# Performance work log

Hardware: AMD Instinct MI355X
Metric: run time of the kernel (lower is better)

The kernel has to match this reference:

```python
import jax, jax.numpy as jnp
import numpy as np
import math

B, NS, NT = 8, 512, 512
NSRC, NTRG = B * NS, B * NT
E = 32768
SCALAR_DIM, EMBED, ORI, LAYERS, K, KK = 20, 128, 1024, 3, 5, 25
CONV_IN = 2 * EMBED
FINAL_IN = ORI + LAYERS * EMBED


def sinusoidal_pos_emb(x):
    half = SCALAR_DIM // 2
    freqs = jnp.exp(-(math.log(10000.0) / (half - 1)) * jnp.arange(half, dtype=x.dtype))
    ang = x[:, None] * freqs[None, :]
    return jnp.concatenate([jnp.sin(ang), jnp.cos(ang)], axis=-1)


def spline_basis(pseudo):
    # open B-spline basis, degree 1, kernel_size K per dim, dim=2 (torch_spline_conv semantics)
    v = pseudo * (K - 1)
    lo = jnp.floor(v)
    frac = v - lo
    lo = lo.astype(jnp.int32)
    idxs, ws = [], []
    for s1 in (0, 1):
        for s0 in (0, 1):
            i0 = jnp.clip(lo[:, 0] + s0, 0, K - 1)
            i1 = jnp.clip(lo[:, 1] + s1, 0, K - 1)
            w0 = frac[:, 0] if s0 else 1.0 - frac[:, 0]
            w1 = frac[:, 1] if s1 else 1.0 - frac[:, 1]
            idxs.append(i0 + K * i1)
            ws.append(w0 * w1)
    idx = jnp.stack(idxs, 1)  # [E,4] kernel indices
    w = jnp.stack(ws, 1)      # [E,4] basis weights
    e = pseudo.shape[0]
    # dense [E,KK] coefficient matrix (<=4 nonzeros per row)
    return jnp.zeros((e, KK), pseudo.dtype).at[jnp.arange(e)[:, None], idx].add(w)


def spline_conv(x, edge_index, edge_attr, W, root, bias):
    # SplineConv(in=CONV_IN, out=EMBED, dim=2, kernel_size=5, degree=1, aggr='mean', root_weight=True)
    src, dst = edge_index[0], edge_index[1]
    x_j = x[src]                    # [E, in] gather of source features
    C = spline_basis(edge_attr)     # [E, KK]
    msg = jnp.zeros((x_j.shape[0], W.shape[-1]), x.dtype)
    for k in range(KK):             # fixed small kernel loop (25 GEMMs)
        msg = msg + (C[:, k:k + 1] * x_j) @ W[k]
    n = x.shape[0]
    agg = jax.ops.segment_sum(msg, dst, num_segments=n)
    deg = jax.ops.segment_sum(jnp.ones((msg.shape[0],), x.dtype), dst, num_segments=n)
    agg = agg / jnp.clip(deg, 1.0)[:, None]   # mean aggregation
    return agg + x @ root + bias


def masked_softmax(src, mask):
    out = jnp.where(mask, src, -jnp.inf)
    out = jax.nn.softmax(out, axis=-1)
    return jnp.where(mask, out, 0.0)


def setup_inputs() -> dict:
    key = jax.random.key(0)
    ks = jax.random.split(key, 16)
    s = 0.02
    # block-diagonal edges: both endpoints within the same graph
    gs = jax.random.randint(ks[11], (E,), 0, B)
    gt = jax.random.randint(ks[12], (E,), 0, B)
    ei_s = jnp.stack([gs * NS + jax.random.randint(ks[13], (E,), 0, NS),
                      gs * NS + jax.random.randint(ks[14], (E,), 0, NS)])
    ei_t = jnp.stack([gt * NT + jax.random.randint(ks[15], (E,), 0, NT),
                      gt * NT + jax.random.randint(ks[0], (E,), 0, NT)])
    return {
        "t": jax.random.uniform(ks[1], (B,)),
        "Xt": jax.random.uniform(ks[2], (B, NS, NT)),
        "x_s": jax.random.normal(ks[3], (NSRC, ORI)),
        "x_t": jax.random.normal(ks[4], (NTRG, ORI)),
        "ea_s": jax.random.uniform(ks[5], (E, 2)),
        "ea_t": jax.random.uniform(ks[6], (E, 2)),
        "lin0_w": jax.random.normal(ks[7], (ORI + 2 * SCALAR_DIM, EMBED)) * s,
        "lin0_b": jnp.zeros((EMBED,)),
        "lin_w": jax.random.normal(ks[8], (LAYERS - 1, EMBED + 2 * SCALAR_DIM, EMBED)) * s,
        "lin_b": jnp.zeros((LAYERS - 1, EMBED)),
        "conv_w": jax.random.normal(ks[9], (LAYERS, KK, CONV_IN, EMBED)) * s,
        "conv_root": jax.random.normal(ks[10], (LAYERS, CONV_IN, EMBED)) * s,
        "conv_bias": jnp.zeros((LAYERS, EMBED)),
        "final_w": jax.random.normal(jax.random.fold_in(key, 99), (FINAL_IN, EMBED)) * s,
        "final_b": jnp.zeros((EMBED,)),
        "ei_s": ei_s,
        "ei_t": ei_t,
        "s_mask": jnp.ones((B, NS), dtype=bool),
        "t_mask": jnp.ones((B, NT), dtype=bool),
        "mask_align": jnp.ones((B, NS, NT), dtype=bool),
    }


def reference(t, Xt, x_s, x_t, ea_s, ea_t, lin0_w, lin0_b, lin_w, lin_b,
              conv_w, conv_root, conv_bias, final_w, final_b,
              ei_s, ei_t, s_mask, t_mask, mask_align):
    # All graphs have exactly NS/NT nodes, so s_mask/t_mask are all-True:
    # boolean select x[s_mask] == reshape, and to_dense_batch == reshape.
    time_emb = sinusoidal_pos_emb(t)                                    # [B, 20]
    num_src = sinusoidal_pos_emb(Xt.sum(-1).reshape(-1) / 10.0)         # [NSRC, 20]
    num_trg = sinusoidal_pos_emb(jnp.swapaxes(Xt, 1, 2).sum(-1).reshape(-1) / 10.0)
    tf_src = jnp.repeat(time_emb, NS, axis=0)                           # per-node time features
    tf_trg = jnp.repeat(time_emb, NT, axis=0)
    xs_src, xs_trg = [x_s], [x_t]
    for i in range(LAYERS):
        w = lin0_w if i == 0 else lin_w[i - 1]
        b = lin0_b if i == 0 else lin_b[i - 1]
        xin_s = jnp.concatenate([xs_src[-1], num_src, tf_src], -1) @ w + b
        xin_t = jnp.concatenate([xs_trg[-1], num_trg, tf_trg], -1) @ w + b
        xp_s = xin_s.reshape(B, NS, EMBED)
        xp_t = xin_t.reshape(B, NT, EMBED)
        tgt_msg = jnp.einsum('bst,btd->bsd', Xt, xp_t)
        src_msg = jnp.einsum('bst,bsd->btd', Xt, xp_s)
        diff_s = (xp_s - tgt_msg).reshape(NSRC, EMBED)
        diff_t = (xp_t - src_msg).reshape(NTRG, EMBED)
        cat_s = jnp.concatenate([xin_s, diff_s], -1)
        cat_t = jnp.concatenate([xin_t, diff_t], -1)
        xs_src.append(jnp.tanh(spline_conv(cat_s, ei_s, ea_s, conv_w[i], conv_root[i], conv_bias[i])))
        xs_trg.append(jnp.tanh(spline_conv(cat_t, ei_t, ea_t, conv_w[i], conv_root[i], conv_bias[i])))
    h_s = jnp.concatenate(xs_src, -1) @ final_w + final_b
    h_t = jnp.concatenate(xs_trg, -1) @ final_w + final_b
    sim = jnp.einsum('bsd,btd->bst', h_s.reshape(B, NS, EMBED), h_t.reshape(B, NT, EMBED))
    return masked_softmax(sim, mask_align).reshape(NSRC, NT)
```

## Files before the change

kernel.cpp:

```cpp
#include <hip/hip_runtime.h>
#include <hip/hip_bf16.h>

typedef __hip_bfloat16 hb;
typedef short short8 __attribute__((ext_vector_type(8)));
typedef float f32x4 __attribute__((ext_vector_type(4)));
typedef unsigned short u16;

#define NNODE 4096
#define NEDGE 32768
#define EMB   128
#define ORI   1024
#define SD    20
#define CIN   256
#define NCV   3328

__device__ __forceinline__ float b2f(hb v){ return __bfloat162float(v); }
__device__ __forceinline__ hb f2b(float v){ return __float2bfloat16(v); }

__device__ __forceinline__ void split2(float x, u16& hi, u16& lo){
  hb h = f2b(x);
  float r = x - b2f(h);
  hb l = f2b(r);
  __builtin_memcpy(&hi, &h, 2);
  __builtin_memcpy(&lo, &l, 2);
}

__device__ __forceinline__ void gl16(const void* g, void* l){
  __builtin_amdgcn_global_load_lds(
      (const __attribute__((address_space(1))) unsigned int*)(size_t)g,
      (__attribute__((address_space(3))) unsigned int*)(unsigned int)(size_t)l,
      16, 0, 0);
}


__global__ __launch_bounds__(256) void k_rowsum(const float* __restrict__ Xt, float* __restrict__ rowsum){
  int row = blockIdx.x*4 + (threadIdx.x >> 6);
  int lane = threadIdx.x & 63;
  const float* p = Xt + (size_t)row*512;
  float s = 0.f;
  for (int i = lane; i < 512; i += 64) s += p[i];
  for (int off = 32; off; off >>= 1) s += __shfl_xor(s, off);
  if (lane == 0) rowsum[row] = s;
}

__global__ __launch_bounds__(256) void k_colsum(const float* __restrict__ Xt, float* __restrict__ colsum){
  int col = blockIdx.x*256 + threadIdx.x;
  int b = col >> 9, t = col & 511;
  const float* p = Xt + (size_t)b*512*512 + t;
  float s = 0.f;
  for (int sidx = 0; sidx < 512; ++sidx) s += p[(size_t)sidx*512];
  colsum[col] = s;
}

__global__ void k_posemb(const float* __restrict__ vals, int n, float scale, float* __restrict__ out){
  int i = blockIdx.x*blockDim.x + threadIdx.x;
  if (i >= n) return;
  float x = vals[i]*scale;
  float c = -logf(10000.f)/9.f;
  for (int j = 0; j < 10; ++j) {
    float f = expf(c*(float)j);
    out[i*20 + j]      = sinf(x*f);
    out[i*20 + 10 + j] = cosf(x*f);
  }
}

__global__ void k_basis2(const float* __restrict__ ea_s, const float* __restrict__ ea_t,
                         int* __restrict__ idx4, float* __restrict__ w4){
  int e = blockIdx.x*256 + threadIdx.x;
  const float* ea = (e < NEDGE) ? ea_s : ea_t;
  int el = e & (NEDGE-1);
  float p0 = ea[el*2]   * 4.0f;
  float p1 = ea[el*2+1] * 4.0f;
  float l0 = floorf(p0), l1 = floorf(p1);
  float f0 = p0 - l0, f1 = p1 - l1;
  int i0 = (int)l0, i1 = (int)l1;
  int j = 0;
  for (int s1 = 0; s1 <= 1; ++s1)
    for (int s0 = 0; s0 <= 1; ++s0) {
      int a  = min(max(i0 + s0, 0), 4);
      int bb = min(max(i1 + s1, 0), 4);
      float w = (s0 ? f0 : 1.f - f0) * (s1 ? f1 : 1.f - f1);
      idx4[e*4 + j] = a + 5*bb;
      w4[e*4 + j] = w;
      ++j;
    }
}

__global__ void k_count2(const int* __restrict__ ds, const int* __restrict__ dt, int* __restrict__ cnt){
  int e = blockIdx.x*256 + threadIdx.x;
  int side = e >= NEDGE;
  int el = e & (NEDGE-1);
  int node = (side ? dt : ds)[el];
  atomicAdd(&cnt[side*NNODE + node], 1);
}

__global__ __launch_bounds__(256) void k_scan2(const int* __restrict__ cntAll, int* __restrict__ rowptrAll,
                                               int* __restrict__ eposAll, float* __restrict__ invAll){
  int sideOff = blockIdx.x*NNODE;
  const int* cnt = cntAll + sideOff;
  int* rowptr = rowptrAll + blockIdx.x*(NNODE+1);
  int* epos = eposAll + sideOff;
  float* inv = invAll + sideOff;
  __shared__ int part[256];
  int tid = threadIdx.x;
  int base = tid*16;
  int v[16]; int s = 0;
  #pragma unroll
  for (int i = 0; i < 16; ++i){
    v[i] = s; int c = cnt[base+i]; s += c;
    inv[base+i] = 1.f / fmaxf((float)c, 1.f);
  }
  part[tid] = s; __syncthreads();
  int total = s;
  for (int off = 1; off < 256; off <<= 1){
    int y = (tid >= off) ? part[tid-off] : 0;
    __syncthreads();
    part[tid] += y;
    __syncthreads();
  }
  int excl = part[tid] - total;
  #pragma unroll
  for (int i = 0; i < 16; ++i){ int r = excl + v[i]; rowptr[base+i] = r; epos[base+i] = r; }
  if (tid == 255) rowptr[4096] = part[255];
}

__global__ void k_fill2(const int* __restrict__ ds, const int* __restrict__ dt,
                        int* __restrict__ eposAll, int* __restrict__ elistAll){
  int e = blockIdx.x*256 + threadIdx.x;
  int side = e >= NEDGE;
  int el = e & (NEDGE-1);
  int node = (side ? dt : ds)[el];
  int p = atomicAdd(&eposAll[side*NNODE + node], 1);
  elistAll[side*NEDGE + p] = el;
}

__global__ __launch_bounds__(256) void k_xtT2(const float* __restrict__ Xt,
    u16* __restrict__ XH, u16* __restrict__ XL, u16* __restrict__ TH, u16* __restrict__ TL){
  __shared__ float tile[64][65];
  int b = blockIdx.z, s0 = blockIdx.y*64, t0 = blockIdx.x*64;
  const float* src = Xt + (size_t)b*262144;
  size_t ob = (size_t)b*262144;
  #pragma unroll 4
  for (int p = 0; p < 16; ++p) {
    int idx = p*256 + threadIdx.x;
    int r = idx >> 6, c = idx & 63;
    float v = src[(size_t)(s0+r)*512 + t0 + c];
    tile[r][c] = v;
    size_t o = ob + (size_t)(s0+r)*512 + t0 + c;
    split2(v, XH[o], XL[o]);
  }
  __syncthreads();
  #pragma unroll 4
  for (int p = 0; p < 16; ++p) {
    int idx = p*256 + threadIdx.x;
    int r = idx >> 6, c = idx & 63;
    float v = tile[c][r];
    size_t o = ob + (size_t)(t0+r)*512 + s0 + c;
    split2(v, TH[o], TL[o]);
  }
}

__global__ void k_wT2(const float* __restrict__ src, u16* __restrict__ dH, u16* __restrict__ dL,
                      int Krows, int ldDst){
  int i = blockIdx.x*256 + threadIdx.x;
  if (i >= 128*ldDst) return;
  int n = i / ldDst, k = i - n*ldDst;
  float v = (k < Krows) ? src[(size_t)k*128 + n] : 0.f;
  split2(v, dH[i], dL[i]);
}

__global__ void k_wc2(const float* __restrict__ convw, const float* __restrict__ root,
                      u16* __restrict__ dH, u16* __restrict__ dL){
  int i = blockIdx.x*256 + threadIdx.x;
  int l = i / (NCV*CIN);
  int r = i - l*(NCV*CIN);
  int k = r & 255, n = r >> 8;
  const float* cw = convw + (size_t)l*25*CIN*128;
  const float* rt = root  + (size_t)l*CIN*128;
  float v;
  if (n < 3200) { int kk = n >> 7, col = n & 127; v = cw[((size_t)kk*256 + k)*128 + col]; }
  else          { int col = n & 127;              v = rt[(size_t)k*128 + col]; }
  split2(v, dH[i], dL[i]);
}

__global__ void k_aux2(const float* __restrict__ nums, const float* __restrict__ numt,
                       const float* __restrict__ temb, u16* __restrict__ aH, u16* __restrict__ aL){
  int i = blockIdx.x*256 + threadIdx.x;
  if (i >= 8192*64) return;
  int r = i >> 6, c = i & 63;
  int side = r >> 12, local = r & 4095, b = (r >> 9) & 7;
  float v = 0.f;
  if (c < 20) v = (side ? numt : nums)[local*20 + c];
  else if (c < 40) v = temb[b*20 + (c - 20)];
  split2(v, aH[i], aL[i]);
}

__global__ __launch_bounds__(256) void k_split(const float* __restrict__ src,
    u16* __restrict__ dH, u16* __restrict__ dL, int n){
  int i = blockIdx.x*256 + threadIdx.x;
  if (i < n) split2(src[i], dH[i], dL[i]);
}

__global__ __launch_bounds__(256) void k_xinT(const float* __restrict__ src,
    u16* __restrict__ dH, u16* __restrict__ dL, float* __restrict__ cat){
  __shared__ float tile[64][65];
  int r0 = blockIdx.x*64, c0 = blockIdx.y*64;
  #pragma unroll 4
  for (int p = 0; p < 16; ++p) {
    int idx = p*256 + threadIdx.x;
    int r = idx >> 6, c = idx & 63;
    float v = src[(size_t)(r0+r)*128 + c0 + c];
    tile[r][c] = v;
    cat[(size_t)(r0+r)*256 + c0 + c]       = v;
    cat[(size_t)(r0+r)*256 + 128 + c0 + c] = v;
  }
  __syncthreads();
  #pragma unroll 4
  for (int p = 0; p < 16; ++p) {
    int idx = p*256 + threadIdx.x;
    int r = idx >> 6, c = idx & 63;
    float v = tile[c][r];
    size_t o = (size_t)(c0+r)*8192 + r0 + c;
    split2(v, dH[o], dL[o]);
  }
}

__global__ __launch_bounds__(256) void k_fillbias(const float* __restrict__ b, float* __restrict__ o){
  int i = blockIdx.x*256 + threadIdx.x;
  o[i] = b[i & 127];
}

__global__ __launch_bounds__(256) void k_gemm(
    const u16* __restrict__ Ah, const u16* __restrict__ Al, int lda, long aBatch,
    const u16* __restrict__ Bh, const u16* __restrict__ Bl, int ldb, long bBatch,
    int K, int flags, int ksplit,
    float* __restrict__ outF, const float* __restrict__ bias,
    int ldo, int oRowOff, int oBatchRows, const float* __restrict__ X,
    const u16* __restrict__ A2h, const u16* __restrict__ A2l,
    const u16* __restrict__ B2h, const u16* __restrict__ B2l, int oRowOff2)
{
  __shared__ __align__(16) u16 S[2][4][4096];
  const int tid = threadIdx.x;
  const int ln = tid & 63, w = tid >> 6;
  const int wm = (w >> 1)*64, wn = (w & 1)*64;
  const int l15 = ln & 15, q = ln >> 4;
  const int by = blockIdx.y;
  int bz = blockIdx.z;
  const u16* Aph = Ah; const u16* Apl = Al;
  const u16* Bph = Bh; const u16* Bpl = Bl;
  int rowOffSel = oRowOff;
  if (B2h != nullptr) {
    int half = gridDim.z >> 1;
    if (bz >= half) { bz -= half; Aph = A2h; Apl = A2l; Bph = B2h; Bpl = B2l; rowOffSel = oRowOff2; }
  }
  const int batch = bz / ksplit;
  const int kidx  = bz - batch*ksplit;
  const int bxm = blockIdx.x;
  const int kSteps = K >> 5;
  const int spc = (kSteps + ksplit - 1) / ksplit;
  const int kBeg = kidx * spc * 32;
  const int kEnd = min(K, kBeg + spc*32);
  if (kBeg >= kEnd) return;
  const u16* Abh = Aph + (size_t)batch*aBatch + (size_t)bxm*128*lda;
  const u16* Abl = Apl + (size_t)batch*aBatch + (size_t)bxm*128*lda;
  const u16* Bbh = Bph + (size_t)batch*bBatch + (size_t)by*128*ldb;
  const u16* Bbl = Bpl + (size_t)batch*bBatch + (size_t)by*128*ldb;

  f32x4 acc[4][4];
  #pragma unroll
  for (int i = 0; i < 4; ++i)
    #pragma unroll
    for (int j = 0; j < 4; ++j) acc[i][j] = (f32x4){0.f,0.f,0.f,0.f};

  const int r0 = w*32 + (ln >> 2);
  const int r1 = r0 + 16;
  const int c0 = ((ln & 3) ^ ((r0 >> 1) & 3)) * 8;
  const int c1 = ((ln & 3) ^ ((r1 >> 1) & 3)) * 8;

  auto stage = [&](int buf, int kc){
    char* wb = (char*)&S[buf][0][0] + w*2048;
    size_t gA0 = (size_t)r0*lda + kc + c0;
    size_t gA1 = (size_t)r1*lda + kc + c1;
    size_t gB0 = (size_t)r0*ldb + kc + c0;
    size_t gB1 = (size_t)r1*ldb + kc + c1;
    gl16(Abh + gA0, wb);           gl16(Abh + gA1, wb + 1024);
    gl16(Abl + gA0, wb + 8192);    gl16(Abl + gA1, wb + 9216);
    gl16(Bbh + gB0, wb + 16384);   gl16(Bbh + gB1, wb + 17408);
    gl16(Bbl + gB0, wb + 24576);   gl16(Bbl + gB1, wb + 25600);
  };

  auto compute = [&](int buf){
    const u16* AhS = &S[buf][0][0]; const u16* AlS = &S[buf][1][0];
    const u16* BhS = &S[buf][2][0]; const u16* BlS = &S[buf][3][0];
    short8 ah[4], al[4], bh[4], bl[4];
    #pragma unroll
    for (int i = 0; i < 4; ++i) {
      int ra = wm + i*16 + l15;
      int oa = ra*32 + ((q ^ ((ra >> 1) & 3)) << 3);
      ah[i] = *(const short8*)&AhS[oa];
      al[i] = *(const short8*)&AlS[oa];
      int rb = wn + i*16 + l15;
      int ob = rb*32 + ((q ^ ((rb >> 1) & 3)) << 3);
      bh[i] = *(const short8*)&BhS[ob];
      bl[i] = *(const short8*)&BlS[ob];
    }
    #pragma unroll
    for (int i = 0; i < 4; ++i)
      #pragma unroll
      for (int j = 0; j < 4; ++j) {
        acc[i][j] = __builtin_amdgcn_mfma_f32_16x16x32_bf16(ah[i], bl[j], acc[i][j], 0, 0, 0);
        acc[i][j] = __builtin_amdgcn_mfma_f32_16x16x32_bf16(al[i], bh[j], acc[i][j], 0, 0, 0);
        acc[i][j] = __builtin_amdgcn_mfma_f32_16x16x32_bf16(ah[i], bh[j], acc[i][j], 0, 0, 0);
      }
  };

  stage(0, kBeg);
  __syncthreads();
  int cur = 0;
  for (int kc = kBeg; kc < kEnd; kc += 32) {
    if (kc + 32 < kEnd) stage(cur ^ 1, kc + 32);
    compute(cur);
    __syncthreads();
    cur ^= 1;
  }

  const int rowBase = rowOffSel + batch*oBatchRows + bxm*128;
  #pragma unroll
  for (int i = 0; i < 4; ++i) {
    #pragma unroll
    for (int j = 0; j < 4; ++j) {
      int col = by*128 + wn + j*16 + l15;
      #pragma unroll
      for (int r = 0; r < 4; ++r) {
        int row = rowBase + wm + i*16 + q*4 + r;
        float v = acc[i][j][r];
        if (flags & 8) {
          if (flags & 4) unsafeAtomicAdd(&outF[(size_t)row*256 + 128 + col], -v);
          else           unsafeAtomicAdd(&outF[(size_t)row*ldo + col], v);
        } else {
          if (flags & 2) v += bias[col];
          if (flags & 1) v += outF[(size_t)row*ldo + col];
          if (flags & 4) {
            float xv = X[(size_t)row*128 + col];
            outF[(size_t)row*256 + col]       = xv;
            outF[(size_t)row*256 + 128 + col] = xv - v;
          } else {
            outF[(size_t)row*ldo + col] = v;
          }
        }
      }
    }
  }
}

__global__ __launch_bounds__(256) void k_aggtanh(const float* __restrict__ Y,
    const int* __restrict__ srcarr, const int* __restrict__ elist, const int* __restrict__ rowptr,
    const int* __restrict__ idx4, const float* __restrict__ w4, const float* __restrict__ inv,
    const float* __restrict__ bias, u16* __restrict__ xsH, u16* __restrict__ xsL){
  int node = blockIdx.x*2 + (threadIdx.x >> 7);
  int tid = threadIdx.x & 127;
  float acc = Y[(size_t)node*NCV + 3200 + tid];
  float wi = inv[node];
  int beg = rowptr[node], end = rowptr[node+1];
  for (int p = beg; p < end; ++p) {
    int e = elist[p];
    int sn = srcarr[e];
    const float* yrow = Y + (size_t)sn*NCV;
    #pragma unroll
    for (int j = 0; j < 4; ++j) {
      int k = idx4[e*4+j];
      float w = w4[e*4+j]*wi;
      acc += w * yrow[k*128 + tid];
    }
  }
  float r = tanhf(acc + bias[tid]);
  split2(r, xsH[(size_t)node*EMB + tid], xsL[(size_t)node*EMB + tid]);
}

__global__ __launch_bounds__(256) void k_softmax(const float* __restrict__ sim, float* __restrict__ out){
  int row = blockIdx.x, tid = threadIdx.x;
  __shared__ float red[8];
  float v0 = sim[(size_t)row*512 + tid];
  float v1 = sim[(size_t)row*512 + 256 + tid];
  int wid = tid >> 6, lane = tid & 63;
  float m = fmaxf(v0, v1);
  for (int off = 32; off; off >>= 1) m = fmaxf(m, __shfl_xor(m, off));
  if (lane == 0) red[wid] = m;
  __syncthreads();
  if (tid == 0) red[4] = fmaxf(fmaxf(red[0], red[1]), fmaxf(red[2], red[3]));
  __syncthreads();
  m = red[4];
  float e0 = expf(v0 - m), e1 = expf(v1 - m);
  float s = e0 + e1;
  for (int off = 32; off; off >>= 1) s += __shfl_xor(s, off);
  if (lane == 0) red[wid] = s;
  __syncthreads();
  if (tid == 0) red[5] = red[0] + red[1] + red[2] + red[3];
  __syncthreads();
  float inv = 1.f / red[5];
  out[(size_t)row*512 + tid]       = e0*inv;
  out[(size_t)row*512 + 256 + tid] = e1*inv;
}


extern "C" void kernel_launch(void* const* d_in, const int* in_sizes, int n_in,
                              void* d_out, int out_size, void* d_ws, size_t ws_size,
                              hipStream_t stream){
  (void)in_sizes; (void)n_in; (void)out_size; (void)ws_size;
  const float* t_in      = (const float*)d_in[0];
  const float* Xt        = (const float*)d_in[1];
  const float* x_s       = (const float*)d_in[2];
  const float* x_t       = (const float*)d_in[3];
  const float* ea_s      = (const float*)d_in[4];
  const float* ea_t      = (const float*)d_in[5];
  const float* lin0_w    = (const float*)d_in[6];
  const float* lin0_b    = (const float*)d_in[7];
  const float* lin_w     = (const float*)d_in[8];
  const float* lin_b     = (const float*)d_in[9];
  const float* conv_w    = (const float*)d_in[10];
  const float* conv_root = (const float*)d_in[11];
  const float* conv_bias = (const float*)d_in[12];
  const float* final_w   = (const float*)d_in[13];
  const float* final_b   = (const float*)d_in[14];
  const int*   ei_s      = (const int*)d_in[15];
  const int*   ei_t      = (const int*)d_in[16];
  float* out = (float*)d_out;

  char* wsb = (char*)d_ws;
  size_t off = 0;
  auto alloc = [&](size_t bytes)->char*{
    char* p = wsb + off;
    off += (bytes + 255) & ~(size_t)255;
    return p;
  };
  float* f_sums  = (float*)alloc(8192*4);
  float* f_temb  = (float*)alloc(8*SD*4);
  float* f_num   = (float*)alloc((size_t)8192*SD*4);
  int*   i_idx   = (int*)  alloc((size_t)2*NEDGE*4*4);
  float* f_w     = (float*)alloc((size_t)2*NEDGE*4*4);
  int*   i_cnt   = (int*)  alloc((size_t)2*NNODE*4);
  float* f_inv   = (float*)alloc((size_t)2*NNODE*4);
  int*   i_rp    = (int*)  alloc((size_t)2*(NNODE+1)*4);
  int*   i_ep    = (int*)  alloc((size_t)2*NNODE*4);
  int*   i_el    = (int*)  alloc((size_t)2*NEDGE*4);
  u16* XtH  = (u16*)alloc((size_t)8*512*512*2);
  u16* XtL  = (u16*)alloc((size_t)8*512*512*2);
  u16* XtTH = (u16*)alloc((size_t)8*512*512*2);
  u16* XtTL = (u16*)alloc((size_t)8*512*512*2);
  u16* w0H  = (u16*)alloc((size_t)128*1088*2);
  u16* w0L  = (u16*)alloc((size_t)128*1088*2);
  u16* w1H  = (u16*)alloc((size_t)128*192*2);
  u16* w1L  = (u16*)alloc((size_t)128*192*2);
  u16* w2H  = (u16*)alloc((size_t)128*192*2);
  u16* w2L  = (u16*)alloc((size_t)128*192*2);
  u16* wfH  = (u16*)alloc((size_t)128*1408*2);
  u16* wfL  = (u16*)alloc((size_t)128*1408*2);
  u16* wcH  = (u16*)alloc((size_t)3*NCV*CIN*2);
  u16* wcL  = (u16*)alloc((size_t)3*NCV*CIN*2);
  u16* auxH = (u16*)alloc((size_t)8192*64*2);
  u16* auxL = (u16*)alloc((size_t)8192*64*2);
  u16* xH   = (u16*)alloc((size_t)8192*1024*2);
  u16* xL   = (u16*)alloc((size_t)8192*1024*2);
  u16* xsH[3]; u16* xsL[3];
  for (int l = 0; l < 3; ++l) {
    xsH[l] = (u16*)alloc((size_t)8192*EMB*2);
    xsL[l] = (u16*)alloc((size_t)8192*EMB*2);
  }
  u16* catH = (u16*)alloc((size_t)8192*CIN*2);
  u16* catL = (u16*)alloc((size_t)8192*CIN*2);
  float* f_xin = (float*)alloc((size_t)8192*EMB*4);
  float* f_cat = (float*)alloc((size_t)8192*CIN*4);
  float* f_Y   = (float*)alloc((size_t)NNODE*NCV*4);
  float* f_sim = f_Y;
  u16* xiTH = (u16*)((char*)f_Y + (size_t)20*1024*1024);
  u16* xiTL = (u16*)((char*)f_Y + (size_t)23*1024*1024);
  u16* hH   = (u16*)((char*)f_Y + (size_t)26*1024*1024);
  u16* hL   = (u16*)((char*)f_Y + (size_t)29*1024*1024);

  auto gemm = [&](const u16* Ahp, const u16* Alp, int lda, long aB,
                  const u16* Bhp, const u16* Blp, int ldb, long bB,
                  int K, int flags, int ksplit, float* o, const float* bias,
                  int ldo, int rowOff, int oBR, const float* X, dim3 grid,
                  const u16* A2h = nullptr, const u16* A2l = nullptr,
                  const u16* B2h = nullptr, const u16* B2l = nullptr, int rowOff2 = 0){
    k_gemm<<<grid, 256, 0, stream>>>(Ahp, Alp, lda, aB, Bhp, Blp, ldb, bB, K, flags, ksplit,
                                     o, bias, ldo, rowOff, oBR, X,
                                     A2h, A2l, B2h, B2l, rowOff2);
  };

  k_xtT2<<<dim3(8,8,8), 256, 0, stream>>>(Xt, XtH, XtL, XtTH, XtTL);
  k_rowsum<<<NNODE/4, 256, 0, stream>>>(Xt, f_sums);
  k_colsum<<<NNODE/256, 256, 0, stream>>>(Xt, f_sums + NNODE);
  k_posemb<<<8192/256, 256, 0, stream>>>(f_sums, 8192, 0.1f, f_num);
  k_posemb<<<1, 64, 0, stream>>>(t_in, 8, 1.0f, f_temb);
  k_aux2<<<(8192*64)/256, 256, 0, stream>>>(f_num, f_num + (size_t)NNODE*SD, f_temb, auxH, auxL);
  k_basis2<<<2*NEDGE/256, 256, 0, stream>>>(ea_s, ea_t, i_idx, f_w);
  hipMemsetAsync(i_cnt, 0, 2*NNODE*4, stream);
  k_count2<<<2*NEDGE/256, 256, 0, stream>>>(ei_s + NEDGE, ei_t + NEDGE, i_cnt);
  k_scan2<<<2, 256, 0, stream>>>(i_cnt, i_rp, i_ep, f_inv);
  k_fill2<<<2*NEDGE/256, 256, 0, stream>>>(ei_s + NEDGE, ei_t + NEDGE, i_ep, i_el);
  k_wT2<<<(128*1088)/256, 256, 0, stream>>>(lin0_w, w0H, w0L, 1064, 1088);
  k_wT2<<<(128*192)/256, 256, 0, stream>>>(lin_w, w1H, w1L, 168, 192);
  k_wT2<<<(128*192)/256, 256, 0, stream>>>(lin_w + (size_t)168*128, w2H, w2L, 168, 192);
  k_wT2<<<(128*1408)/256, 256, 0, stream>>>(final_w, wfH, wfL, 1408, 1408);
  k_wc2<<<(3*NCV*CIN)/256, 256, 0, stream>>>(conv_w, conv_root, wcH, wcL);
  k_split<<<(4096*1024)/256, 256, 0, stream>>>(x_s, xH, xL, 4096*1024);
  k_split<<<(4096*1024)/256, 256, 0, stream>>>(x_t, xH + (size_t)4096*1024, xL + (size_t)4096*1024, 4096*1024);

  for (int i = 0; i < 3; ++i) {
    const u16* wTh = (i == 0) ? w0H : (i == 1) ? w1H : w2H;
    const u16* wTl = (i == 0) ? w0L : (i == 1) ? w1L : w2L;
    const float* bv = (i == 0) ? lin0_b : lin_b + (i-1)*EMB;
    int ldw = (i == 0) ? 1088 : 192;
    int Kx  = (i == 0) ? 1024 : 128;

    gemm(auxH, auxL, 64, 0, wTh + Kx, wTl + Kx, ldw, 0,
         64, 2, 1, f_xin, bv, EMB, 0, 0, nullptr, dim3(64,1,1));
    const u16* A0h = (i == 0) ? xH : xsH[i-1];
    const u16* A0l = (i == 0) ? xL : xsL[i-1];
    int ks = (i == 0) ? 8 : 4;
    gemm(A0h, A0l, Kx, 0, wTh, wTl, ldw, 0,
         Kx, 8, ks, f_xin, nullptr, EMB, 0, 0, nullptr, dim3(64,1,ks));

    k_xinT<<<dim3(128,2), 256, 0, stream>>>(f_xin, xiTH, xiTL, f_cat);
    gemm(XtH, XtL, 512, 262144, xiTH + 4096, xiTL + 4096, 8192, 512,
         512, 4|8, 8, f_cat, nullptr, 256, 0, 512, nullptr, dim3(4,1,128),
         XtTH, XtTL, xiTH, xiTL, NNODE);
    k_split<<<(8192*CIN)/256, 256, 0, stream>>>(f_cat, catH, catL, 8192*CIN);

    for (int side = 0; side < 2; ++side) {
      gemm(catH + (size_t)side*NNODE*CIN, catL + (size_t)side*NNODE*CIN, CIN, 0,
           wcH + (size_t)i*NCV*CIN, wcL + (size_t)i*NCV*CIN, CIN, 0,
           CIN, 0, 1, f_Y, nullptr, NCV, 0, 0, nullptr, dim3(32,26,1));
      k_aggtanh<<<NNODE/2, 256, 0, stream>>>(f_Y,
          side ? ei_t : ei_s, i_el + side*NEDGE, i_rp + side*(NNODE+1),
          i_idx + (size_t)side*NEDGE*4, f_w + (size_t)side*NEDGE*4, f_inv + side*NNODE,
          conv_bias + i*EMB,
          xsH[i] + (size_t)side*NNODE*EMB, xsL[i] + (size_t)side*NNODE*EMB);
    }
  }

  float* f_h = f_xin;
  k_fillbias<<<4096, 256, 0, stream>>>(final_b, f_h);
  gemm(xH, xL, 1024, 0, wfH, wfL, 1408, 0,
       1024, 8, 8, f_h, nullptr, EMB, 0, 0, nullptr, dim3(64,1,8));
  for (int l = 0; l < 3; ++l)
    gemm(xsH[l], xsL[l], 128, 0, wfH + 1024 + l*128, wfL + 1024 + l*128, 1408, 0,
         128, 8, 4, f_h, nullptr, EMB, 0, 0, nullptr, dim3(64,1,4));
  k_split<<<(8192*EMB)/256, 256, 0, stream>>>(f_h, hH, hL, 8192*EMB);

  hipMemsetAsync(f_sim, 0, (size_t)4096*512*4, stream);
  gemm(hH, hL, EMB, 65536, hH + (size_t)4096*EMB, hL + (size_t)4096*EMB, EMB, 65536,
       EMB, 8, 4, f_sim, nullptr, 512, 0, 512, nullptr, dim3(4,4,32));

  k_softmax<<<NNODE, 256, 0, stream>>>(f_sim, out);
}
```

Before: 949.4 us.

## Store spline-conv GEMM output as bf16 and batch both sides in one launch

The per-kernel spline GEMM now writes its output Y as bf16 rather than fp32, which halves the write and gather traffic. Both graph sides now run in a single GEMM launch over a z-dimension of 2 and a single aggregation kernel that picks the side from the node index. Rounding Y to plain bf16 drops the hi/lo split precision the rest of the pipeline keeps, so accuracy may suffer. The merged launches remove two launches per layer and expose more parallelism.

```diff
diff --git a/kernel.cpp b/kernel.cpp
--- a/kernel.cpp
+++ b/kernel.cpp
@@ -16,6 +16,7 @@
 
 __device__ __forceinline__ float b2f(hb v){ return __bfloat162float(v); }
 __device__ __forceinline__ hb f2b(float v){ return __float2bfloat16(v); }
+__device__ __forceinline__ float u2f(u16 u){ hb h; __builtin_memcpy(&h, &u, 2); return b2f(h); }
 
 __device__ __forceinline__ void split2(float x, u16& hi, u16& lo){
   hb h = f2b(x);
@@ -334,7 +335,11 @@
       for (int r = 0; r < 4; ++r) {
         int row = rowBase + wm + i*16 + q*4 + r;
         float v = acc[i][j][r];
-        if (flags & 8) {
+        if (flags & 16) {
+          hb hv = f2b(v);
+          u16 uv; __builtin_memcpy(&uv, &hv, 2);
+          ((u16*)outF)[(size_t)row*ldo + col] = uv;
+        } else if (flags & 8) {
           if (flags & 4) unsafeAtomicAdd(&outF[(size_t)row*256 + 128 + col], -v);
           else           unsafeAtomicAdd(&outF[(size_t)row*ldo + col], v);
         } else {
@@ -353,28 +358,37 @@
   }
 }
 
-__global__ __launch_bounds__(256) void k_aggtanh(const float* __restrict__ Y,
-    const int* __restrict__ srcarr, const int* __restrict__ elist, const int* __restrict__ rowptr,
-    const int* __restrict__ idx4, const float* __restrict__ w4, const float* __restrict__ inv,
-    const float* __restrict__ bias, u16* __restrict__ xsH, u16* __restrict__ xsL){
-  int node = blockIdx.x*2 + (threadIdx.x >> 7);
+__global__ __launch_bounds__(256) void k_aggtanh(const u16* __restrict__ Y,
+    const int* __restrict__ src_s, const int* __restrict__ src_t,
+    const int* __restrict__ elistAll, const int* __restrict__ rowptrAll,
+    const int* __restrict__ idx4All, const float* __restrict__ w4All,
+    const float* __restrict__ invAll, const float* __restrict__ biasAll, int layer,
+    u16* __restrict__ xsH, u16* __restrict__ xsL){
+  int n = blockIdx.x*2 + (threadIdx.x >> 7);
   int tid = threadIdx.x & 127;
-  float acc = Y[(size_t)node*NCV + 3200 + tid];
-  float wi = inv[node];
-  int beg = rowptr[node], end = rowptr[node+1];
+  int side = n >> 12, local = n & 4095;
+  const int* srcarr = side ? src_t : src_s;
+  const int* elist  = elistAll + side*NEDGE;
+  const int* rowptr = rowptrAll + side*(NNODE+1);
+  const int* idx4   = idx4All + (size_t)side*NEDGE*4;
+  const float* w4   = w4All + (size_t)side*NEDGE*4;
+  const u16* Yb = Y + (size_t)side*NNODE*NCV;
+  float acc = u2f(Yb[(size_t)local*NCV + 3200 + tid]);
+  float wi = invAll[side*NNODE + local];
+  int beg = rowptr[local], end = rowptr[local+1];
   for (int p = beg; p < end; ++p) {
     int e = elist[p];
     int sn = srcarr[e];
-    const float* yrow = Y + (size_t)sn*NCV;
+    const u16* yrow = Yb + (size_t)sn*NCV;
     #pragma unroll
     for (int j = 0; j < 4; ++j) {
       int k = idx4[e*4+j];
       float w = w4[e*4+j]*wi;
-      acc += w * yrow[k*128 + tid];
+      acc += w * u2f(yrow[k*128 + tid]);
     }
   }
-  float r = tanhf(acc + bias[tid]);
-  split2(r, xsH[(size_t)node*EMB + tid], xsL[(size_t)node*EMB + tid]);
+  float r = tanhf(acc + biasAll[layer*EMB + tid]);
+  split2(r, xsH[(size_t)n*EMB + tid], xsL[(size_t)n*EMB + tid]);
 }
 
 __global__ __launch_bounds__(256) void k_softmax(const float* __restrict__ sim, float* __restrict__ out){
@@ -470,8 +484,8 @@
   u16* catL = (u16*)alloc((size_t)8192*CIN*2);
   float* f_xin = (float*)alloc((size_t)8192*EMB*4);
   float* f_cat = (float*)alloc((size_t)8192*CIN*4);
-  float* f_Y   = (float*)alloc((size_t)NNODE*NCV*4);
-  float* f_sim = f_Y;
+  u16*   f_Y   = (u16*)  alloc((size_t)8192*NCV*2);
+  float* f_sim = (float*)f_Y;
   u16* xiTH = (u16*)((char*)f_Y + (size_t)20*1024*1024);
   u16* xiTL = (u16*)((char*)f_Y + (size_t)23*1024*1024);
   u16* hH   = (u16*)((char*)f_Y + (size_t)26*1024*1024);
@@ -528,16 +542,13 @@
          XtTH, XtTL, xiTH, xiTL, NNODE);
     k_split<<<(8192*CIN)/256, 256, 0, stream>>>(f_cat, catH, catL, 8192*CIN);
 
-    for (int side = 0; side < 2; ++side) {
-      gemm(catH + (size_t)side*NNODE*CIN, catL + (size_t)side*NNODE*CIN, CIN, 0,
-           wcH + (size_t)i*NCV*CIN, wcL + (size_t)i*NCV*CIN, CIN, 0,
-           CIN, 0, 1, f_Y, nullptr, NCV, 0, 0, nullptr, dim3(32,26,1));
-      k_aggtanh<<<NNODE/2, 256, 0, stream>>>(f_Y,
-          side ? ei_t : ei_s, i_el + side*NEDGE, i_rp + side*(NNODE+1),
-          i_idx + (size_t)side*NEDGE*4, f_w + (size_t)side*NEDGE*4, f_inv + side*NNODE,
-          conv_bias + i*EMB,
-          xsH[i] + (size_t)side*NNODE*EMB, xsL[i] + (size_t)side*NNODE*EMB);
-    }
+    gemm(catH, catL, CIN, 0,
+         wcH + (size_t)i*NCV*CIN, wcL + (size_t)i*NCV*CIN, CIN, 0,
+         CIN, 16, 1, (float*)f_Y, nullptr, NCV, 0, 0, nullptr, dim3(32,26,2),
+         catH + (size_t)NNODE*CIN, catL + (size_t)NNODE*CIN,
+         wcH + (size_t)i*NCV*CIN, wcL + (size_t)i*NCV*CIN, NNODE);
+    k_aggtanh<<<4096, 256, 0, stream>>>(f_Y, ei_s, ei_t, i_el, i_rp,
+        i_idx, f_w, f_inv, conv_bias, i, xsH[i], xsL[i]);
   }
 
   float* f_h = f_xin;
```

New measurement: 864.1 us. 9.0% less time.
